# Kernel tuning notes

Measured on AMD Instinct MI355X. Metric: run time of the kernel, lower is better.

The kernel has to match this reference:

```python
import jax, jax.numpy as jnp
import numpy as np


def _build_levels():
    # build_power_value(B=4): w_bit=5 -> B=4 additive-powers-of-two codebook
    value_a = [0.0] + [2.0 ** (-2 * i - 1) for i in range(3)]
    value_b = [0.0] + [2.0 ** (-2 * i - 2) for i in range(3)]
    sums = sorted({a + b for a in value_a for b in value_b})
    levels = np.asarray(sums, dtype=np.float32)
    return jnp.asarray(levels / levels.max())  # 16 levels in [0, 1]


def setup_inputs() -> dict:
    key = jax.random.key(0)
    weight = jax.random.normal(key, (4096, 4096), dtype=jnp.float32) * 0.05
    wgt_alpha = jnp.asarray(2.0, dtype=jnp.float32)
    return {"weight": weight, "wgt_alpha": wgt_alpha}


def reference(weight, wgt_alpha):
    levels = _build_levels()
    # stats are computed on weight.data in torch (detached)
    mean = jax.lax.stop_gradient(jnp.mean(weight))
    std = jax.lax.stop_gradient(jnp.std(weight, ddof=1))  # torch .std() is unbiased
    wn = (weight - mean) / std
    x = wn / wgt_alpha
    xc = jnp.clip(x, -1.0, 1.0)
    sign = jnp.sign(xc)
    # nearest-level search over the 16-entry codebook (first-min tie-break like torch)
    idx = jnp.argmin(jnp.abs(jnp.abs(xc)[..., None] - levels), axis=-1)
    q = levels[idx] * sign
    return q * wgt_alpha
```

## Files before the change

### kernel.cpp

```cpp
#include <hip/hip_runtime.h>
#include <math.h>

#define THREADS 256

typedef float f2v __attribute__((ext_vector_type(2)));
typedef float f4v __attribute__((ext_vector_type(4)));

static constexpr float kLvl[16] = {
    0.0f      / 0.75f, 0.015625f / 0.75f, 0.03125f / 0.75f, 0.046875f / 0.75f,
    0.0625f   / 0.75f, 0.09375f  / 0.75f, 0.125f   / 0.75f, 0.140625f / 0.75f,
    0.1875f   / 0.75f, 0.25f     / 0.75f, 0.28125f / 0.75f, 0.375f    / 0.75f,
    0.5f      / 0.75f, 0.515625f / 0.75f, 0.5625f  / 0.75f, 0.75f     / 0.75f,
};
static constexpr double kMid[15] = {
    ((double)kLvl[0]  + (double)kLvl[1])  * 0.5, ((double)kLvl[1]  + (double)kLvl[2])  * 0.5,
    ((double)kLvl[2]  + (double)kLvl[3])  * 0.5, ((double)kLvl[3]  + (double)kLvl[4])  * 0.5,
    ((double)kLvl[4]  + (double)kLvl[5])  * 0.5, ((double)kLvl[5]  + (double)kLvl[6])  * 0.5,
    ((double)kLvl[6]  + (double)kLvl[7])  * 0.5, ((double)kLvl[7]  + (double)kLvl[8])  * 0.5,
    ((double)kLvl[8]  + (double)kLvl[9])  * 0.5, ((double)kLvl[9]  + (double)kLvl[10]) * 0.5,
    ((double)kLvl[10] + (double)kLvl[11]) * 0.5, ((double)kLvl[11] + (double)kLvl[12]) * 0.5,
    ((double)kLvl[12] + (double)kLvl[13]) * 0.5, ((double)kLvl[13] + (double)kLvl[14]) * 0.5,
    ((double)kLvl[14] + (double)kLvl[15]) * 0.5,
};

__device__ __forceinline__ float tree64(float v) {
    #pragma unroll
    for (int m = 1; m <= 32; m <<= 1)
        v += __shfl_xor(v, m, 64);
    return v;
}

__device__ __forceinline__ float sgpr_bcast(float x) {
    return __uint_as_float(__builtin_amdgcn_readfirstlane(__float_as_uint(x)));
}

#define QSEL(V, RES) do {                                   \
    float _u  = (V) - mean;                                 \
    float _au = fabsf(_u);                                  \
    float _o  = c0;                                         \
    _o = (_au < t0)  ? _o : c1;                             \
    _o = (_au < t1)  ? _o : c2;                             \
    _o = (_au < t2)  ? _o : c3;                             \
    _o = (_au < t3)  ? _o : c4;                             \
    _o = (_au < t4)  ? _o : c5;                             \
    _o = (_au < t5)  ? _o : c6;                             \
    _o = (_au < t6)  ? _o : c7;                             \
    _o = (_au < t7)  ? _o : c8;                             \
    _o = (_au < t8)  ? _o : c9;                             \
    _o = (_au < t9)  ? _o : c10;                            \
    _o = (_au < t10) ? _o : c11;                            \
    _o = (_au < t11) ? _o : c12;                            \
    _o = (_au < t12) ? _o : c13;                            \
    _o = (_au < t13) ? _o : c14;                            \
    _o = (_au < t14) ? _o : c15;                            \
    RES = copysignf(_o, _u);                                \
} while (0)

#define HOIST_TC()                                                        \
    const float t0  = sgpr_bcast(sT[0]),  t1  = sgpr_bcast(sT[1]);        \
    const float t2  = sgpr_bcast(sT[2]),  t3  = sgpr_bcast(sT[3]);        \
    const float t4  = sgpr_bcast(sT[4]),  t5  = sgpr_bcast(sT[5]);        \
    const float t6  = sgpr_bcast(sT[6]),  t7  = sgpr_bcast(sT[7]);        \
    const float t8  = sgpr_bcast(sT[8]),  t9  = sgpr_bcast(sT[9]);        \
    const float t10 = sgpr_bcast(sT[10]), t11 = sgpr_bcast(sT[11]);       \
    const float t12 = sgpr_bcast(sT[12]), t13 = sgpr_bcast(sT[13]);       \
    const float t14 = sgpr_bcast(sT[14]);                                 \
    const float c0  = sgpr_bcast(sC[0]),  c1  = sgpr_bcast(sC[1]);        \
    const float c2  = sgpr_bcast(sC[2]),  c3  = sgpr_bcast(sC[3]);        \
    const float c4  = sgpr_bcast(sC[4]),  c5  = sgpr_bcast(sC[5]);        \
    const float c6  = sgpr_bcast(sC[6]),  c7  = sgpr_bcast(sC[7]);        \
    const float c8  = sgpr_bcast(sC[8]),  c9  = sgpr_bcast(sC[9]);        \
    const float c10 = sgpr_bcast(sC[10]), c11 = sgpr_bcast(sC[11]);       \
    const float c12 = sgpr_bcast(sC[12]), c13 = sgpr_bcast(sC[13]);       \
    const float c14 = sgpr_bcast(sC[14]), c15 = sgpr_bcast(sC[15]);

#define THRESH_SETUP(TID)                                                 \
    if ((TID) < 15) {                                                     \
        const double mid = kMid[(TID)];                                   \
        unsigned lo = 0u, hi = 0x7F800000u;                               \
        while (lo < hi) {                                                 \
            unsigned m = (lo + hi) >> 1;                                  \
            float uu = __uint_as_float(m);                                \
            float y  = uu / sd;                                           \
            float x  = y / al;                                            \
            float xc = fminf(x, 1.0f);                                    \
            if ((double)xc > mid) hi = m; else lo = m + 1;                \
        }                                                                 \
        sT[(TID)] = __uint_as_float(lo);                                  \
    } else if ((TID) < 31) {                                              \
        sC[(TID) - 15] = kLvl[(TID) - 15] * al;                           \
    } else if ((TID) == 31) {                                             \
        sC[0] = 0.0f;                                                     \
    }

template<int PASS, int REV>
__global__ __launch_bounds__(THREADS) void leaf_pass(const float* __restrict__ w,
                                                     const float* __restrict__ bprev,
                                                     float* __restrict__ bout,
                                                     long long n, int nb) {
    #pragma clang fp contract(off)
    __shared__ float ws4[4];
    __shared__ float smean;
    float mean = 0.0f;
    if (PASS == 1) {
        int i0 = threadIdx.x * 8;
        float v = 0.0f;
        if (i0 + 7 < nb) {
            const float* p = bprev + i0;
            v = ((p[0] + p[1]) + (p[2] + p[3])) + ((p[4] + p[5]) + (p[6] + p[7]));
        }
        v = tree64(v);
        if ((threadIdx.x & 63) == 0) ws4[threadIdx.x >> 6] = v;
        __syncthreads();
        if (threadIdx.x == 0)
            smean = ((ws4[0] + ws4[1]) + (ws4[2] + ws4[3])) / (float)n;
        __syncthreads();
        mean = smean;
    }
    int region = blockIdx.x;
    if (REV && (nb & 7) == 0) {
        int j = blockIdx.x >> 3;
        region = (blockIdx.x & 7) + 8 * ((nb >> 3) - 1 - j);
    }
    const long long base = (long long)region * 8192
                         + (long long)(threadIdx.x >> 2) * 128
                         + (long long)(threadIdx.x & 3) * 2;
    const f2v* p = (const f2v*)(w + base);
    float s0, s1;
    {
        f2v a = p[0];
        if (PASS == 1) { float x = a.x - mean, y = a.y - mean; s0 = x * x; s1 = y * y; }
        else           { s0 = a.x; s1 = a.y; }
    }
    #pragma unroll
    for (int t = 1; t < 16; ++t) {
        f2v a = p[4 * t];
        if (PASS == 1) { float x = a.x - mean, y = a.y - mean; s0 += x * x; s1 += y * y; }
        else           { s0 += a.x; s1 += a.y; }
    }
    float s = s0 + s1;
    s = tree64(s);
    if ((threadIdx.x & 63) == 0) ws4[threadIdx.x >> 6] = s;
    __syncthreads();
    if (threadIdx.x == 0)
        bout[region] = (ws4[0] + ws4[1]) + (ws4[2] + ws4[3]);
}

__global__ __launch_bounds__(THREADS) void quantize_b(const f4v* __restrict__ w4,
                                                      f4v* __restrict__ o4,
                                                      const float* __restrict__ bout0,
                                                      const float* __restrict__ bout1,
                                                      const float* __restrict__ alpha_ptr,
                                                      long long n, int nb) {
    #pragma clang fp contract(off)
    __shared__ float wsA[4], wsB[4];
    __shared__ float sP[2];
    __shared__ float sT[15];
    __shared__ float sC[16];
    {
        int i0 = threadIdx.x * 8;
        float v = 0.0f, u = 0.0f;
        if (i0 + 7 < nb) {
            const float* p0 = bout0 + i0;
            const float* p1 = bout1 + i0;
            v = ((p0[0] + p0[1]) + (p0[2] + p0[3])) + ((p0[4] + p0[5]) + (p0[6] + p0[7]));
            u = ((p1[0] + p1[1]) + (p1[2] + p1[3])) + ((p1[4] + p1[5]) + (p1[6] + p1[7]));
        }
        v = tree64(v);
        u = tree64(u);
        if ((threadIdx.x & 63) == 0) { wsA[threadIdx.x >> 6] = v; wsB[threadIdx.x >> 6] = u; }
        __syncthreads();
        if (threadIdx.x == 0) {
            sP[0] = ((wsA[0] + wsA[1]) + (wsA[2] + wsA[3])) / (float)n;
            sP[1] = sqrtf(((wsB[0] + wsB[1]) + (wsB[2] + wsB[3])) / (float)(n - 1));
        }
        __syncthreads();
    }
    {
        const float sd = sP[1];
        const float al = alpha_ptr[0];
        THRESH_SETUP(threadIdx.x)
    }
    __syncthreads();

    const float mean = sgpr_bcast(sP[0]);
    HOIST_TC()

    const long long base = (long long)blockIdx.x * 2048 + threadIdx.x;
    f4v a0 = w4[base];
    f4v a1 = w4[base + 256];
    f4v a2 = w4[base + 512];
    f4v a3 = w4[base + 768];
    f4v a4 = w4[base + 1024];
    f4v a5 = w4[base + 1280];
    f4v a6 = w4[base + 1536];
    f4v a7 = w4[base + 1792];
    f4v r;
    QSEL(a0.x, r.x); QSEL(a0.y, r.y); QSEL(a0.z, r.z); QSEL(a0.w, r.w);
    __builtin_nontemporal_store(r, &o4[base]);
    QSEL(a1.x, r.x); QSEL(a1.y, r.y); QSEL(a1.z, r.z); QSEL(a1.w, r.w);
    __builtin_nontemporal_store(r, &o4[base + 256]);
    QSEL(a2.x, r.x); QSEL(a2.y, r.y); QSEL(a2.z, r.z); QSEL(a2.w, r.w);
    __builtin_nontemporal_store(r, &o4[base + 512]);
    QSEL(a3.x, r.x); QSEL(a3.y, r.y); QSEL(a3.z, r.z); QSEL(a3.w, r.w);
    __builtin_nontemporal_store(r, &o4[base + 768]);
    QSEL(a4.x, r.x); QSEL(a4.y, r.y); QSEL(a4.z, r.z); QSEL(a4.w, r.w);
    __builtin_nontemporal_store(r, &o4[base + 1024]);
    QSEL(a5.x, r.x); QSEL(a5.y, r.y); QSEL(a5.z, r.z); QSEL(a5.w, r.w);
    __builtin_nontemporal_store(r, &o4[base + 1280]);
    QSEL(a6.x, r.x); QSEL(a6.y, r.y); QSEL(a6.z, r.z); QSEL(a6.w, r.w);
    __builtin_nontemporal_store(r, &o4[base + 1536]);
    QSEL(a7.x, r.x); QSEL(a7.y, r.y); QSEL(a7.z, r.z); QSEL(a7.w, r.w);
    __builtin_nontemporal_store(r, &o4[base + 1792]);
}

__global__ __launch_bounds__(THREADS) void quantize_g(const f4v* __restrict__ w4,
                                                      f4v* __restrict__ o4,
                                                      const float* __restrict__ bout0,
                                                      const float* __restrict__ bout1,
                                                      const float* __restrict__ alpha_ptr,
                                                      long long n, int nb) {
    #pragma clang fp contract(off)
    __shared__ float wsA[4], wsB[4];
    __shared__ float sP[2];
    __shared__ float sT[15];
    __shared__ float sC[16];
    {
        int i0 = threadIdx.x * 8;
        float v = 0.0f, u = 0.0f;
        if (i0 + 7 < nb) {
            const float* p0 = bout0 + i0;
            const float* p1 = bout1 + i0;
            v = ((p0[0] + p0[1]) + (p0[2] + p0[3])) + ((p0[4] + p0[5]) + (p0[6] + p0[7]));
            u = ((p1[0] + p1[1]) + (p1[2] + p1[3])) + ((p1[4] + p1[5]) + (p1[6] + p1[7]));
        }
        v = tree64(v);
        u = tree64(u);
        if ((threadIdx.x & 63) == 0) { wsA[threadIdx.x >> 6] = v; wsB[threadIdx.x >> 6] = u; }
        __syncthreads();
        if (threadIdx.x == 0) {
            sP[0] = ((wsA[0] + wsA[1]) + (wsA[2] + wsA[3])) / (float)n;
            sP[1] = sqrtf(((wsB[0] + wsB[1]) + (wsB[2] + wsB[3])) / (float)(n - 1));
        }
        __syncthreads();
    }
    {
        const float sd = sP[1];
        const float al = alpha_ptr[0];
        THRESH_SETUP(threadIdx.x)
    }
    __syncthreads();

    const float mean = sgpr_bcast(sP[0]);
    HOIST_TC()

    long long n4     = n >> 2;
    long long tid    = (long long)blockIdx.x * THREADS + threadIdx.x;
    long long stride = (long long)gridDim.x * THREADS;
    long long i = tid;
    for (; i + stride < n4; i += 2 * stride) {
        f4v a = w4[i];
        f4v b = w4[i + stride];
        f4v ra, rb;
        QSEL(a.x, ra.x); QSEL(a.y, ra.y); QSEL(a.z, ra.z); QSEL(a.w, ra.w);
        QSEL(b.x, rb.x); QSEL(b.y, rb.y); QSEL(b.z, rb.z); QSEL(b.w, rb.w);
        __builtin_nontemporal_store(ra, &o4[i]);
        __builtin_nontemporal_store(rb, &o4[i + stride]);
    }
    for (; i < n4; i += stride) {
        f4v a = w4[i];
        f4v ra;
        QSEL(a.x, ra.x); QSEL(a.y, ra.y); QSEL(a.z, ra.z); QSEL(a.w, ra.w);
        __builtin_nontemporal_store(ra, &o4[i]);
    }
}

extern "C" void kernel_launch(void* const* d_in, const int* in_sizes, int n_in,
                              void* d_out, int out_size, void* d_ws, size_t ws_size,
                              hipStream_t stream) {
    const float* w     = (const float*)d_in[0];
    const float* alpha = (const float*)d_in[1];
    float* out = (float*)d_out;
    long long n = (long long)in_sizes[0];

    int nblk = (int)(n >> 13);
    float* bout0 = (float*)d_ws;
    float* bout1 = bout0 + nblk;

    leaf_pass<0, 0><<<nblk, THREADS, 0, stream>>>(w, nullptr, bout0, n, nblk);
    leaf_pass<1, 1><<<nblk, THREADS, 0, stream>>>(w, bout0, bout1, n, nblk);
    if (n == (1LL << 24)) {
        quantize_b<<<nblk, THREADS, 0, stream>>>((const f4v*)w, (f4v*)out,
                                                 bout0, bout1, alpha, n, nblk);
    } else {
        quantize_g<<<2048, THREADS, 0, stream>>>((const f4v*)w, (f4v*)out,
                                                 bout0, bout1, alpha, n, nblk);
    }
}
```

Baseline: 52.70 us.

## Replace 15-compare select chain with bucketed LDS lookup table in quantize_b

Per-element quantization in quantize_b switches from a 15-step compare/select chain to a 128-bucket lookup table in shared memory. Each bucket holds at most one threshold and the two candidate codes, so one multiply, one clamp, one LDS vector load and one compare replace the chain. This cuts ALU work per element, but adds per-block table construction, two extra barriers, and LDS reads that may bank-conflict. Correctness relies on no bucket containing more than one threshold.

```diff
diff --git a/kernel.cpp b/kernel.cpp
--- a/kernel.cpp
+++ b/kernel.cpp
@@ -56,6 +56,16 @@
     RES = copysignf(_o, _u);                                \
 } while (0)
 
+#define QTAB(V, RES) do {                                            \
+    float _u  = (V) - mean;                                          \
+    float _au = __uint_as_float(__float_as_uint(_u) & 0x7fffffffu);  \
+    unsigned _i = (unsigned)(_au * invH);                            \
+    _i = _i > 127u ? 127u : _i;                                      \
+    f4v _e = *(const f4v*)&tbl[_i][0];                               \
+    float _o = (_au < _e.x) ? _e.y : _e.z;                           \
+    RES = copysignf(_o, _u);                                         \
+} while (0)
+
 #define HOIST_TC()                                                        \
     const float t0  = sgpr_bcast(sT[0]),  t1  = sgpr_bcast(sT[1]);        \
     const float t2  = sgpr_bcast(sT[2]),  t3  = sgpr_bcast(sT[3]);        \
@@ -157,6 +167,8 @@
     __shared__ float sP[2];
     __shared__ float sT[15];
     __shared__ float sC[16];
+    __shared__ float sInvH;
+    __shared__ float tbl[128][4];
     {
         int i0 = threadIdx.x * 8;
         float v = 0.0f, u = 0.0f;
@@ -182,9 +194,30 @@
         THRESH_SETUP(threadIdx.x)
     }
     __syncthreads();
+    if (threadIdx.x == 0) sInvH = 120.0f / sT[14];
+    __syncthreads();
+    const float invH = sgpr_bcast(sInvH);
+    if (threadIdx.x < 128) {
+        const int b = threadIdx.x;
+        int base = 0;
+        float Tq = __builtin_inff();
+        #pragma unroll
+        for (int k = 0; k < 15; ++k) {
+            float Tk = sT[k];
+            unsigned bk = (unsigned)(Tk * invH);
+            bk = bk > 127u ? 127u : bk;
+            if (bk < (unsigned)b) base++;
+            if (bk == (unsigned)b) Tq = Tk;
+        }
+        int hi = base + 1 <= 15 ? base + 1 : 15;
+        tbl[b][0] = Tq;
+        tbl[b][1] = sC[base];
+        tbl[b][2] = sC[hi];
+        tbl[b][3] = 0.0f;
+    }
+    __syncthreads();
 
     const float mean = sgpr_bcast(sP[0]);
-    HOIST_TC()
 
     const long long base = (long long)blockIdx.x * 2048 + threadIdx.x;
     f4v a0 = w4[base];
@@ -196,21 +229,21 @@
     f4v a6 = w4[base + 1536];
     f4v a7 = w4[base + 1792];
     f4v r;
-    QSEL(a0.x, r.x); QSEL(a0.y, r.y); QSEL(a0.z, r.z); QSEL(a0.w, r.w);
+    QTAB(a0.x, r.x); QTAB(a0.y, r.y); QTAB(a0.z, r.z); QTAB(a0.w, r.w);
     __builtin_nontemporal_store(r, &o4[base]);
-    QSEL(a1.x, r.x); QSEL(a1.y, r.y); QSEL(a1.z, r.z); QSEL(a1.w, r.w);
+    QTAB(a1.x, r.x); QTAB(a1.y, r.y); QTAB(a1.z, r.z); QTAB(a1.w, r.w);
     __builtin_nontemporal_store(r, &o4[base + 256]);
-    QSEL(a2.x, r.x); QSEL(a2.y, r.y); QSEL(a2.z, r.z); QSEL(a2.w, r.w);
+    QTAB(a2.x, r.x); QTAB(a2.y, r.y); QTAB(a2.z, r.z); QTAB(a2.w, r.w);
     __builtin_nontemporal_store(r, &o4[base + 512]);
-    QSEL(a3.x, r.x); QSEL(a3.y, r.y); QSEL(a3.z, r.z); QSEL(a3.w, r.w);
+    QTAB(a3.x, r.x); QTAB(a3.y, r.y); QTAB(a3.z, r.z); QTAB(a3.w, r.w);
     __builtin_nontemporal_store(r, &o4[base + 768]);
-    QSEL(a4.x, r.x); QSEL(a4.y, r.y); QSEL(a4.z, r.z); QSEL(a4.w, r.w);
+    QTAB(a4.x, r.x); QTAB(a4.y, r.y); QTAB(a4.z, r.z); QTAB(a4.w, r.w);
     __builtin_nontemporal_store(r, &o4[base + 1024]);
-    QSEL(a5.x, r.x); QSEL(a5.y, r.y); QSEL(a5.z, r.z); QSEL(a5.w, r.w);
+    QTAB(a5.x, r.x); QTAB(a5.y, r.y); QTAB(a5.z, r.z); QTAB(a5.w, r.w);
     __builtin_nontemporal_store(r, &o4[base + 1280]);
-    QSEL(a6.x, r.x); QSEL(a6.y, r.y); QSEL(a6.z, r.z); QSEL(a6.w, r.w);
+    QTAB(a6.x, r.x); QTAB(a6.y, r.y); QTAB(a6.z, r.z); QTAB(a6.w, r.w);
     __builtin_nontemporal_store(r, &o4[base + 1536]);
-    QSEL(a7.x, r.x); QSEL(a7.y, r.y); QSEL(a7.z, r.z); QSEL(a7.w, r.w);
+    QTAB(a7.x, r.x); QTAB(a7.y, r.y); QTAB(a7.z, r.z); QTAB(a7.w, r.w);
     __builtin_nontemporal_store(r, &o4[base + 1792]);
 }
 
```

After: 46.24 us, median of 2. -12.3%, faster.
